# Kernel tuning notes

Hardware: AMD Instinct MI355X
Metric: run time of the kernel (lower is better)

Reference implementation:

```python
import jax, jax.numpy as jnp
import numpy as np

MAX_H = 22
NUM_HEADS = 8
EPS = 1e-5
SLOPE = 0.01  # torch LeakyReLU default


def setup_inputs() -> dict:
    key = jax.random.key(0)
    ks = jax.random.split(key, 8)
    n, c, s, h, w = 16, 64, 30, 64, 22
    cp, v = 64, 17
    p, out_c = 7, 256
    D = c * MAX_H + cp * 2  # fuse_dim = 1536
    sil = jax.random.normal(ks[0], (n, c, s, h, w), dtype=jnp.float32)
    pose = jax.random.normal(ks[1], (n, cp, s, v), dtype=jnp.float32)
    min_idx = jax.random.randint(ks[2], (p, n), 0, h - MAX_H + 1, dtype=jnp.int32)
    max_idx = min_idx + MAX_H  # slices are exactly MAX_H rows (static shape)
    fc_bin = jax.random.normal(ks[3], (p, D, out_c), dtype=jnp.float32) * np.sqrt(2.0 / (D + out_c))
    gamma = 1.0 + 0.1 * jax.random.normal(ks[4], (out_c,), dtype=jnp.float32)
    beta = 0.1 * jax.random.normal(ks[5], (out_c,), dtype=jnp.float32)
    w_qkv = jax.random.normal(ks[6], (3 * out_c, out_c), dtype=jnp.float32) * 0.02
    w_proj = jax.random.normal(ks[7], (out_c, out_c), dtype=jnp.float32) * 0.02
    return {"sil": sil, "pose": pose, "fc_bin": fc_bin, "gamma": gamma, "beta": beta,
            "w_qkv": w_qkv, "w_proj": w_proj, "min_idx": min_idx, "max_idx": max_idx}


def _forward(sil, pose, fc_bin, gamma, beta, w_qkv, w_proj, min_idx):
    n, c, s, h, w = sil.shape
    p = min_idx.shape[0]
    sil_p = jnp.transpose(sil, (0, 2, 1, 3, 4))  # [n,s,c,h,w]
    parts = []
    for j in range(p):  # fixed small part loop; each gather is a big vectorized op
        idx = min_idx[j][:, None] + jnp.arange(MAX_H, dtype=min_idx.dtype)  # [n,MAX_H]
        g = jnp.take_along_axis(sil_p, idx[:, None, None, :, None], axis=3)  # [n,s,c,MAX_H,w]
        parts.append(g.mean(-1) + g.max(-1))  # mean + max pool over width
    silpart = jnp.stack(parts, 0)  # [p,n,s,c,MAX_H]
    silpart = jnp.transpose(silpart, (1, 2, 0, 3, 4)).reshape(n * s, p, c * MAX_H)

    cp, v = pose.shape[1], pose.shape[3]
    pose_r = jnp.transpose(pose, (0, 2, 1, 3)).reshape(n * s, cp, v)  # [ns,cp,17]
    # part 0: AdaptiveAvgPool1d(2) on 5 joints -> mean(j0..j2), mean(j2..j4)
    part0 = jnp.stack([pose_r[:, :, 0:3].mean(-1), pose_r[:, :, 2:5].mean(-1)], -1)  # [ns,cp,2]
    # parts 1..6: pairs of joints, pool(2->2) is identity
    others = pose_r[:, :, 5:].reshape(n * s, cp, 6, 2).transpose(0, 2, 1, 3)  # [ns,6,cp,2]
    posepart = jnp.concatenate([part0[:, None], others], axis=1)  # [ns,p,cp,2]
    posepart = jax.nn.leaky_relu(posepart, SLOPE).reshape(n * s, p, cp * 2)

    fuse = jnp.concatenate([silpart, posepart], axis=2)  # [ns,p,D]
    x = jnp.einsum('npd,pdo->npo', fuse, fc_bin)  # per-part FC -> [ns,p,out]

    # BatchNorm1d (training-mode batch stats) over [ns,out,p]
    x = jnp.transpose(x, (0, 2, 1))  # [ns,out,p]
    mu = x.mean((0, 2), keepdims=True)
    var = x.var((0, 2), keepdims=True)
    x = (x - mu) * jax.lax.rsqrt(var + EPS) * gamma[None, :, None] + beta[None, :, None]
    x = jnp.transpose(x, (0, 2, 1))  # [ns,p,out]

    # Attention over the p part tokens (note: source softmaxes over the HEAD axis)
    B, N, C = x.shape
    hd = C // NUM_HEADS
    qkv = (x @ w_qkv.T).reshape(B, N, 3, NUM_HEADS, hd).transpose(2, 0, 3, 1, 4)
    q, k, vv = qkv[0], qkv[1], qkv[2]  # [B,H,N,hd]
    attn = jnp.einsum('bhnd,bhmd->bhnm', q, k) * (hd ** -0.5)
    attn = jax.nn.softmax(attn, axis=1)  # faithful to attn.softmax(dim=1)
    ao = jnp.einsum('bhnm,bhmd->bhnd', attn, vv).transpose(0, 2, 1, 3).reshape(B, N, C)
    x = x + ao @ w_proj.T

    return x.reshape(n, s, p, C).transpose(0, 3, 1, 2)  # [n,out,s,p]


def reference(sil, pose, fc_bin, gamma, beta, w_qkv, w_proj, min_idx, max_idx):
    # max_idx == min_idx + MAX_H by construction; slice length is static MAX_H
    return _forward(sil, pose, fc_bin, gamma, beta, w_qkv, w_proj, min_idx)
```

## Files before the change

### kernel.cpp

```cpp
#include <hip/hip_runtime.h>
#include <hip/hip_bf16.h>
#include <math.h>

#define NS 480
#define NN 16
#define SS 30
#define CC 64
#define HHH 64
#define WW 22
#define PP 7
#define MAXH 22
#define CP 64
#define VV 17
#define DD 1536
#define OC 256
#define SILD 1408
#define NTOK 3360
#define LDQ 776

typedef __bf16 bf16x8 __attribute__((ext_vector_type(8)));
typedef float f32x4 __attribute__((ext_vector_type(4)));
typedef short short8 __attribute__((ext_vector_type(8)));

__device__ __forceinline__ void gl_lds16(const void* g, void* l) {
    __builtin_amdgcn_global_load_lds(
        (const __attribute__((address_space(1))) void*)g,
        (__attribute__((address_space(3))) void*)l, 16, 0, 0);
}

__device__ __forceinline__ float bf2f(short s) {
    union { float f; unsigned u; } uu; uu.u = ((unsigned)(unsigned short)s) << 16; return uu.f;
}

__global__ __launch_bounds__(256) void prep(const float* __restrict__ sil,
                                            const int* __restrict__ min_idx,
                                            const float* __restrict__ wqkv,
                                            const float* __restrict__ wproj,
                                            const float* __restrict__ fcbin,
                                            const float* __restrict__ pose,
                                            __hip_bfloat16* __restrict__ fuse,
                                            __hip_bfloat16* __restrict__ wqkv16,
                                            __hip_bfloat16* __restrict__ wproj16,
                                            __hip_bfloat16* __restrict__ fcbinT16) {
    __shared__ __align__(16) char smem[47552];
    int b = blockIdx.x, tid = threadIdx.x;
    if (b < 3840) {
        float* lds  = (float*)smem;
        float* hbuf = (float*)(smem + 45056);
        int*   mi_s = (int*)(smem + 47104);
        if (tid < 112) mi_s[tid] = min_idx[tid];
        long long base = (long long)b * 11264;
        int w = tid >> 6, lane = tid & 63;
        const char* gsrc = (const char*)(sil + base) + lane * 16;
        #pragma unroll
        for (int i = 0; i < 11; i++) {
            int ci = w * 11 + i;
            gl_lds16(gsrc + ci * 1024, (char*)smem + ci * 1024);
        }
        __syncthreads();
        #pragma unroll
        for (int rr = 0; rr < 2; rr++) {
            int r = tid + rr * 256;
            const float* row = lds + r * 22;
            float s = 0.f, m = -INFINITY;
            #pragma unroll
            for (int k = 0; k < WW; k++) { float v = row[k]; s += v; m = fmaxf(m, v); }
            hbuf[r] = s * (1.0f / WW) + m;
        }
        __syncthreads();
        int q0 = b * 8;
        for (int idx = tid; idx < 8 * PP * MAXH; idx += 256) {
            int hh = idx % MAXH;
            int t2 = idx / MAXH;
            int j = t2 % PP, qi = t2 / PP;
            int q = q0 + qi;
            int s_i = q % SS, t3 = q / SS;
            int c = t3 & 63, n = t3 >> 6;
            int mi = mi_s[j * NN + n];
            fuse[((long long)(j * NS + n * SS + s_i)) * DD + c * MAXH + hh] =
                __float2bfloat16(hbuf[qi * 64 + mi + hh]);
        }
        return;
    }
    b -= 3840;
    if (b < 768)  { int g = b * 256 + tid; wqkv16[g] = __float2bfloat16(wqkv[g]); return; }
    if (b < 1024) { int g = (b - 768) * 256 + tid; wproj16[g] = __float2bfloat16(wproj[g]); return; }
    if (b < 1696) {
        float (*t)[65] = (float(*)[65])smem;
        int bb = b - 1024;
        int p = bb / 96, r2 = bb % 96, dt = r2 / 4, ot = r2 % 4;
        const float* s = fcbin + ((long long)p * DD + dt * 64) * OC + ot * 64;
        for (int i = tid; i < 64 * 64; i += 256) {
            int r = i >> 6, c = i & 63;
            t[r][c] = s[(long long)r * OC + c];
        }
        __syncthreads();
        __hip_bfloat16* d = fcbinT16 + ((long long)p * OC + ot * 64) * DD + dt * 64;
        for (int i = tid; i < 64 * 64; i += 256) {
            int r = i >> 6, c = i & 63;
            d[(long long)r * DD + c] = __float2bfloat16(t[c][r]);
        }
        return;
    }
    int g = (b - 1696) * 256 + tid;
    int dd = g & 127;
    int t2 = g >> 7;
    int nsi = t2 % NS;
    int j = t2 / NS;
    int n = nsi / SS, s_i = nsi % SS;
    int cpi = dd >> 1, par = dd & 1;
    const float* pr = pose + (((long long)n * CP + cpi) * SS + s_i) * VV;
    float v;
    if (j == 0) {
        v = (par == 0) ? (pr[0] + pr[1] + pr[2]) * (1.f / 3.f)
                       : (pr[2] + pr[3] + pr[4]) * (1.f / 3.f);
    } else {
        v = pr[5 + (j - 1) * 2 + par];
    }
    v = (v > 0.f) ? v : 0.01f * v;
    fuse[(long long)(j * NS + nsi) * DD + SILD + dd] = __float2bfloat16(v);
}

__global__ __launch_bounds__(512) void gemm_fc(
    const __hip_bfloat16* __restrict__ Ain, const __hip_bfloat16* __restrict__ Bt,
    float* __restrict__ Cf, float* __restrict__ partial)
{
    const int M = 480, K = 1536, lda = 1536, ldc = 1792;
    const __hip_bfloat16* Ab = Ain + (long long)blockIdx.z * 480 * 1536;
    const __hip_bfloat16* Bq = Bt + (long long)blockIdx.z * 256 * 1536;
    float* C = Cf + (long long)blockIdx.z * 256;

    __shared__ short As[2][2][4096];
    __shared__ short Bs[2][2][4096];
    __shared__ float red[4][2][16][2];

    int tid = threadIdx.x, lane = tid & 63, w = tid >> 6;
    int kg = w >> 2, wq = w & 3;
    int wm = wq >> 1, wn = wq & 1;
    int row0 = blockIdx.x * 64, col0 = blockIdx.y * 64;
    int kbase = kg * 768;

    f32x4 acc[2][2] = {};

    auto stage = [&](int buf, int k0) {
        int cc = lane & 7;
        #pragma unroll
        for (int i = 0; i < 2; i++) {
            int r = wq * 16 + i * 8 + (lane >> 3);
            int grow = row0 + r; if (grow >= M) grow = M - 1;
            long long kk = kbase + k0;
            const char* ga = (const char*)Ab + (((long long)grow * lda + kk) << 1) + ((cc ^ (r & 7)) << 4);
            gl_lds16(ga, (char*)&As[kg][buf][0] + (wq * 16 + i * 8) * 128);
            const char* gb = (const char*)Bq + (((long long)(col0 + r) * K + kk) << 1) + ((cc ^ (r & 7)) << 4);
            gl_lds16(gb, (char*)&Bs[kg][buf][0] + (wq * 16 + i * 8) * 128);
        }
    };

    stage(0, 0);
    __syncthreads();
    for (int t = 0; t < 12; t++) {
        int cur = t & 1;
        if (t + 1 < 12) stage(cur ^ 1, (t + 1) << 6);
        #pragma unroll
        for (int ks = 0; ks < 2; ks++) {
            bf16x8 af[2], bfv[2];
            #pragma unroll
            for (int f = 0; f < 2; f++) {
                int r = wm * 32 + f * 16 + (lane & 15);
                int ca = (ks * 4 + (lane >> 4)) ^ (r & 7);
                af[f] = *(const bf16x8*)((const char*)&As[kg][cur][0] + r * 128 + (ca << 4));
                int rb = wn * 32 + f * 16 + (lane & 15);
                int cb = (ks * 4 + (lane >> 4)) ^ (rb & 7);
                bfv[f] = *(const bf16x8*)((const char*)&Bs[kg][cur][0] + rb * 128 + (cb << 4));
            }
            #pragma unroll
            for (int fm = 0; fm < 2; fm++)
                #pragma unroll
                for (int fn = 0; fn < 2; fn++)
                    acc[fm][fn] = __builtin_amdgcn_mfma_f32_16x16x32_bf16(
                        af[fm], bfv[fn], acc[fm][fn], 0, 0, 0);
        }
        __syncthreads();
    }

    float* redC = (float*)&As[0][0][0];
    if (kg == 1) {
        #pragma unroll
        for (int fm = 0; fm < 2; fm++)
            #pragma unroll
            for (int fn = 0; fn < 2; fn++)
                #pragma unroll
                for (int r4 = 0; r4 < 4; r4++) {
                    int rl = wm * 32 + fm * 16 + (lane >> 4) * 4 + r4;
                    int cl = wn * 32 + fn * 16 + (lane & 15);
                    redC[rl * 64 + cl] = acc[fm][fn][r4];
                }
    }
    __syncthreads();

    if (kg == 0) {
        float s[2] = {0.f, 0.f}, s2[2] = {0.f, 0.f};
        #pragma unroll
        for (int fm = 0; fm < 2; fm++) {
            #pragma unroll
            for (int fn = 0; fn < 2; fn++) {
                #pragma unroll
                for (int r4 = 0; r4 < 4; r4++) {
                    int rl = wm * 32 + fm * 16 + (lane >> 4) * 4 + r4;
                    int cl = wn * 32 + fn * 16 + (lane & 15);
                    int grow = row0 + rl;
                    if (grow < M) {
                        float v = acc[fm][fn][r4] + redC[rl * 64 + cl];
                        C[(long long)grow * ldc + col0 + cl] = v;
                        s[fn] += v; s2[fn] += v * v;
                    }
                }
            }
        }
        #pragma unroll
        for (int off = 16; off < 64; off <<= 1) {
            s[0] += __shfl_xor(s[0], off);  s2[0] += __shfl_xor(s2[0], off);
            s[1] += __shfl_xor(s[1], off);  s2[1] += __shfl_xor(s2[1], off);
        }
        if (lane < 16) {
            red[wq][0][lane][0] = s[0]; red[wq][0][lane][1] = s2[0];
            red[wq][1][lane][0] = s[1]; red[wq][1][lane][1] = s2[1];
        }
    }
    __syncthreads();
    if (tid < 128) {
        int col = tid >> 1, which = tid & 1;
        int wn2 = (col >> 5) & 1, fn2 = (col >> 4) & 1, c16 = col & 15;
        float v = red[wn2][fn2][c16][which] + red[2 + wn2][fn2][c16][which];
        partial[((long long)(blockIdx.z * 8 + blockIdx.x) * 2 + which) * 256 + blockIdx.y * 64 + col] = v;
    }
}

__global__ __launch_bounds__(256) void bnfinal(const float* __restrict__ partial,
                                               const float* __restrict__ gamma,
                                               const float* __restrict__ beta,
                                               float* __restrict__ ssbuf) {
    int t = threadIdx.x;
    float s = 0.f, s2 = 0.f;
    #pragma unroll 8
    for (int b = 0; b < 56; b++) { s += partial[b * 512 + t]; s2 += partial[b * 512 + 256 + t]; }
    float mu = s / (float)NTOK;
    float var = s2 / (float)NTOK - mu * mu;
    float rsig = rsqrtf(var + 1e-5f);
    float sc = gamma[t] * rsig;
    ssbuf[t] = sc;
    ssbuf[256 + t] = beta[t] - mu * sc;
}

__global__ __launch_bounds__(256) void gemm_qkv(
    const float* __restrict__ xraw, const __hip_bfloat16* __restrict__ Bt,
    const float* __restrict__ ssb, __hip_bfloat16* __restrict__ qkv16)
{
    const int M = 3360, K = 256;
    __shared__ short As[2][4096];
    __shared__ short Bs[2][4096];
    __shared__ float ssl[512];
    int tid = threadIdx.x, lane = tid & 63, w = tid >> 6;
    int wm = w >> 1, wn = w & 1;
    int row0 = blockIdx.x * 64, col0 = blockIdx.y * 64;

    for (int i = tid; i < 512; i += 256) ssl[i] = ssb[i];
    __syncthreads();

    f32x4 acc[2][2] = {};

    auto stageB = [&](int buf, int k0) {
        int cc = lane & 7;
        #pragma unroll
        for (int i = 0; i < 2; i++) {
            int r = w * 16 + i * 8 + (lane >> 3);
            const char* gb = (const char*)Bt + (((long long)(col0 + r) * K + k0) << 1) + ((cc ^ (r & 7)) << 4);
            gl_lds16(gb, (char*)&Bs[buf][0] + (w * 16 + i * 8) * 128);
        }
    };
    auto stageA = [&](int buf, int k0) {
        #pragma unroll
        for (int i = 0; i < 2; i++) {
            int id = tid + i * 256;
            int r = id >> 3, c8 = id & 7;
            int grow = row0 + r; if (grow >= M) grow = M - 1;
            const float* src = xraw + (long long)grow * 256 + k0 + c8 * 8;
            float4 v0 = *(const float4*)src;
            float4 v1 = *(const float4*)(src + 4);
            int kb = k0 + c8 * 8;
            float vv[8] = {v0.x, v0.y, v0.z, v0.w, v1.x, v1.y, v1.z, v1.w};
            short8 o;
            #pragma unroll
            for (int j = 0; j < 8; j++) {
                float tv = vv[j] * ssl[kb + j] + ssl[256 + kb + j];
                union { __hip_bfloat16 h; short s; } u; u.h = __float2bfloat16(tv);
                o[j] = u.s;
            }
            *(short8*)((char*)&As[buf][0] + r * 128 + ((c8 ^ (r & 7)) << 4)) = o;
        }
    };

    stageA(0, 0); stageB(0, 0);
    __syncthreads();
    for (int t = 0; t < 4; t++) {
        int cur = t & 1;
        if (t + 1 < 4) { stageA(cur ^ 1, (t + 1) << 6); stageB(cur ^ 1, (t + 1) << 6); }
        #pragma unroll
        for (int ks = 0; ks < 2; ks++) {
            bf16x8 af[2], bfv[2];
            #pragma unroll
            for (int f = 0; f < 2; f++) {
                int r = wm * 32 + f * 16 + (lane & 15);
                int ca = (ks * 4 + (lane >> 4)) ^ (r & 7);
                af[f] = *(const bf16x8*)((const char*)&As[cur][0] + r * 128 + (ca << 4));
                int rb = wn * 32 + f * 16 + (lane & 15);
                int cb = (ks * 4 + (lane >> 4)) ^ (rb & 7);
                bfv[f] = *(const bf16x8*)((const char*)&Bs[cur][0] + rb * 128 + (cb << 4));
            }
            #pragma unroll
            for (int fm = 0; fm < 2; fm++)
                #pragma unroll
                for (int fn = 0; fn < 2; fn++)
                    acc[fm][fn] = __builtin_amdgcn_mfma_f32_16x16x32_bf16(
                        af[fm], bfv[fn], acc[fm][fn], 0, 0, 0);
        }
        __syncthreads();
    }
    #pragma unroll
    for (int fm = 0; fm < 2; fm++)
        #pragma unroll
        for (int fn = 0; fn < 2; fn++)
            #pragma unroll
            for (int r4 = 0; r4 < 4; r4++) {
                int grow = row0 + wm * 32 + fm * 16 + (lane >> 4) * 4 + r4;
                int gcol = col0 + wn * 32 + fn * 16 + (lane & 15);
                if (grow < M)
                    qkv16[(long long)grow * 768 + gcol] = __float2bfloat16(acc[fm][fn][r4]);
            }
}

__global__ __launch_bounds__(256) void attnproj(const __hip_bfloat16* __restrict__ qkv16,
                                                const __hip_bfloat16* __restrict__ wproj16,
                                                const float* __restrict__ xraw,
                                                const float* __restrict__ ssb,
                                                float* __restrict__ outp) {
    __shared__ __align__(16) char sm[33728];
    float* qkvs = (float*)sm;
    float* Ct   = (float*)sm;
    short* ao_s = (short*)(sm + 21728);
    float (*as_)[49] = (float(*)[49])(sm + 29920);
    float* ssl  = (float*)(sm + 31680);

    int tid = threadIdx.x, lane = tid & 63, w = tid >> 6;
    int token0 = blockIdx.x * 7;

    for (int i = tid; i < 512; i += 256) ssl[i] = ssb[i];

    const short* src = (const short*)qkv16 + (long long)token0 * 768;
    for (int c = tid; c < 672; c += 256) {
        int r = c / 96, c8 = (c % 96) * 8;
        short8 v = *(const short8*)(src + r * 768 + c8);
        float4 f0, f1;
        f0.x = bf2f(v[0]); f0.y = bf2f(v[1]); f0.z = bf2f(v[2]); f0.w = bf2f(v[3]);
        f1.x = bf2f(v[4]); f1.y = bf2f(v[5]); f1.z = bf2f(v[6]); f1.w = bf2f(v[7]);
        *(float4*)&qkvs[r * LDQ + c8] = f0;
        *(float4*)&qkvs[r * LDQ + c8 + 4] = f1;
    }
    __syncthreads();

    for (int t = tid; t < 392; t += 256) {
        int h = t / 49, ij = t % 49, i = ij / 7, j = ij % 7;
        const float* qp = qkvs + i * LDQ + h * 32;
        const float* kp = qkvs + j * LDQ + 256 + h * 32;
        float acc = 0.f;
        #pragma unroll
        for (int d = 0; d < 32; d++) acc += qp[d] * kp[d];
        as_[h][ij] = acc * 0.17677669529663689f;
    }
    __syncthreads();
    if (tid < 49) {
        float m = -INFINITY;
        #pragma unroll
        for (int h = 0; h < 8; h++) m = fmaxf(m, as_[h][tid]);
        float e[8], sum = 0.f;
        #pragma unroll
        for (int h = 0; h < 8; h++) { e[h] = __expf(as_[h][tid] - m); sum += e[h]; }
        float inv = 1.f / sum;
        #pragma unroll
        for (int h = 0; h < 8; h++) as_[h][tid] = e[h] * inv;
    }
    __syncthreads();
    #pragma unroll
    for (int tl = 0; tl < 16; tl++) {
        int col = tid;
        float acc = 0.f;
        if (tl < 7) {
            int h = col >> 5;
            const float* ap = &as_[h][tl * 7];
            const float* vp = qkvs + 512 + col;
            #pragma unroll
            for (int j = 0; j < 7; j++) acc += ap[j] * vp[j * LDQ];
        }
        int c16 = col >> 3;
        union { __hip_bfloat16 h2; short s2; } u; u.h2 = __float2bfloat16(acc);
        ao_s[tl * 256 + ((c16 ^ (tl & 7)) << 3) + (col & 7)] = u.s2;
    }
    __syncthreads();
    f32x4 pacc[4] = {};
    int n0 = w * 64;
    #pragma unroll
    for (int k0 = 0; k0 < 256; k0 += 32) {
        int rowa = lane & 15;
        int kk = k0 + (lane >> 4) * 8;
        int c16a = kk >> 3;
        bf16x8 af = *(const bf16x8*)(const void*)&ao_s[rowa * 256 + ((c16a ^ (rowa & 7)) << 3)];
        #pragma unroll
        for (int fn = 0; fn < 4; fn++) {
            int n = n0 + fn * 16 + (lane & 15);
            bf16x8 bfv = *(const bf16x8*)(const void*)((const short*)wproj16 + n * 256 + kk);
            pacc[fn] = __builtin_amdgcn_mfma_f32_16x16x32_bf16(af, bfv, pacc[fn], 0, 0, 0);
        }
    }
    __syncthreads();
    #pragma unroll
    for (int fn = 0; fn < 4; fn++)
        #pragma unroll
        for (int r4 = 0; r4 < 4; r4++) {
            int tk = (lane >> 4) * 4 + r4;
            if (tk < 7) {
                int o = n0 + fn * 16 + (lane & 15);
                Ct[o * 9 + tk] = pacc[fn][r4];
            }
        }
    __syncthreads();
    int o = tid;
    int n = token0 / 210, rem0 = token0 % 210;
    float* op = outp + ((long long)(n * 256 + o)) * 210 + rem0;
    float sc = ssl[o], sh = ssl[256 + o];
    #pragma unroll
    for (int tk = 0; tk < 7; tk++) {
        op[tk] = Ct[o * 9 + tk] + xraw[(long long)(token0 + tk) * 256 + o] * sc + sh;
    }
}

extern "C" void kernel_launch(void* const* d_in, const int* in_sizes, int n_in,
                              void* d_out, int out_size, void* d_ws, size_t ws_size,
                              hipStream_t stream) {
    const float* sil   = (const float*)d_in[0];
    const float* pose  = (const float*)d_in[1];
    const float* fcbin = (const float*)d_in[2];
    const float* gamma = (const float*)d_in[3];
    const float* beta  = (const float*)d_in[4];
    const float* wqkv  = (const float*)d_in[5];
    const float* wproj = (const float*)d_in[6];
    const int*   minidx= (const int*)d_in[7];
    float* out = (float*)d_out;

    float* ws = (float*)d_ws;
    __hip_bfloat16* fuse16   = (__hip_bfloat16*)ws;
    float* xraw    = ws + 2580480;
    float* partial = ws + 3440640;
    float* ssbuf   = ws + 3469312;
    __hip_bfloat16* wqkv16   = (__hip_bfloat16*)(ws + 3469824);
    __hip_bfloat16* wproj16  = (__hip_bfloat16*)(ws + 3568128);
    __hip_bfloat16* fcbinT16 = (__hip_bfloat16*)(ws + 3600896);
    __hip_bfloat16* qkv16    = (__hip_bfloat16*)(ws + 4977152);

    prep<<<7216, 256, 0, stream>>>(sil, minidx, wqkv, wproj, fcbin, pose,
                                   fuse16, wqkv16, wproj16, fcbinT16);
    gemm_fc<<<dim3(8, 4, 7), 512, 0, stream>>>(fuse16, fcbinT16, xraw, partial);
    bnfinal<<<1, 256, 0, stream>>>(partial, gamma, beta, ssbuf);
    gemm_qkv<<<dim3(53, 12), 256, 0, stream>>>(xraw, wqkv16, ssbuf, qkv16);
    attnproj<<<480, 256, 0, stream>>>(qkv16, wproj16, xraw, ssbuf, out);
}
```

Baseline: 81.43 us.

## Fold BN finalize into QKV GEMM and remap FC GEMM blocks across XCDs

Removes the single-block bnfinal kernel launch. Every gemm_qkv block now reduces the 56 partial BN sums itself to build its scale/shift table, and block (0,0) writes it to global memory for attnproj. The FC GEMM launch is flattened to a 1D grid with a remapped block index, likely so that blocks sharing a part's weights land on the same XCD's L2. The cost is redundant partial-sum reads in all 636 QKV blocks.

```diff
diff --git a/kernel.cpp b/kernel.cpp
--- a/kernel.cpp
+++ b/kernel.cpp
@@ -126,9 +126,15 @@
     float* __restrict__ Cf, float* __restrict__ partial)
 {
     const int M = 480, K = 1536, lda = 1536, ldc = 1792;
-    const __hip_bfloat16* Ab = Ain + (long long)blockIdx.z * 480 * 1536;
-    const __hip_bfloat16* Bq = Bt + (long long)blockIdx.z * 256 * 1536;
-    float* C = Cf + (long long)blockIdx.z * 256;
+    int bid = blockIdx.x;
+    int v = (bid & 7) * 28 + (bid >> 3);
+    int bz = v >> 5;
+    int rem = v & 31;
+    int by = rem >> 3, bx = rem & 7;
+
+    const __hip_bfloat16* Ab = Ain + (long long)bz * 480 * 1536;
+    const __hip_bfloat16* Bq = Bt + (long long)bz * 256 * 1536;
+    float* C = Cf + (long long)bz * 256;
 
     __shared__ short As[2][2][4096];
     __shared__ short Bs[2][2][4096];
@@ -137,7 +143,7 @@
     int tid = threadIdx.x, lane = tid & 63, w = tid >> 6;
     int kg = w >> 2, wq = w & 3;
     int wm = wq >> 1, wn = wq & 1;
-    int row0 = blockIdx.x * 64, col0 = blockIdx.y * 64;
+    int row0 = bx * 64, col0 = by * 64;
     int kbase = kg * 768;
 
     f32x4 acc[2][2] = {};
@@ -210,9 +216,9 @@
                     int cl = wn * 32 + fn * 16 + (lane & 15);
                     int grow = row0 + rl;
                     if (grow < M) {
-                        float v = acc[fm][fn][r4] + redC[rl * 64 + cl];
-                        C[(long long)grow * ldc + col0 + cl] = v;
-                        s[fn] += v; s2[fn] += v * v;
+                        float vv = acc[fm][fn][r4] + redC[rl * 64 + cl];
+                        C[(long long)grow * ldc + col0 + cl] = vv;
+                        s[fn] += vv; s2[fn] += vv * vv;
                     }
                 }
             }
@@ -231,30 +237,16 @@
     if (tid < 128) {
         int col = tid >> 1, which = tid & 1;
         int wn2 = (col >> 5) & 1, fn2 = (col >> 4) & 1, c16 = col & 15;
-        float v = red[wn2][fn2][c16][which] + red[2 + wn2][fn2][c16][which];
-        partial[((long long)(blockIdx.z * 8 + blockIdx.x) * 2 + which) * 256 + blockIdx.y * 64 + col] = v;
-    }
-}
-
-__global__ __launch_bounds__(256) void bnfinal(const float* __restrict__ partial,
-                                               const float* __restrict__ gamma,
-                                               const float* __restrict__ beta,
-                                               float* __restrict__ ssbuf) {
-    int t = threadIdx.x;
-    float s = 0.f, s2 = 0.f;
-    #pragma unroll 8
-    for (int b = 0; b < 56; b++) { s += partial[b * 512 + t]; s2 += partial[b * 512 + 256 + t]; }
-    float mu = s / (float)NTOK;
-    float var = s2 / (float)NTOK - mu * mu;
-    float rsig = rsqrtf(var + 1e-5f);
-    float sc = gamma[t] * rsig;
-    ssbuf[t] = sc;
-    ssbuf[256 + t] = beta[t] - mu * sc;
+        float vv = red[wn2][fn2][c16][which] + red[2 + wn2][fn2][c16][which];
+        partial[((long long)(bz * 8 + bx) * 2 + which) * 256 + by * 64 + col] = vv;
+    }
 }
 
 __global__ __launch_bounds__(256) void gemm_qkv(
     const float* __restrict__ xraw, const __hip_bfloat16* __restrict__ Bt,
-    const float* __restrict__ ssb, __hip_bfloat16* __restrict__ qkv16)
+    const float* __restrict__ partial, const float* __restrict__ gamma,
+    const float* __restrict__ beta, float* __restrict__ ssbuf,
+    __hip_bfloat16* __restrict__ qkv16)
 {
     const int M = 3360, K = 256;
     __shared__ short As[2][4096];
@@ -264,7 +256,25 @@
     int wm = w >> 1, wn = w & 1;
     int row0 = blockIdx.x * 64, col0 = blockIdx.y * 64;
 
-    for (int i = tid; i < 512; i += 256) ssl[i] = ssb[i];
+    {
+        float s = 0.f, s2 = 0.f;
+        #pragma unroll 8
+        for (int bb = 0; bb < 56; bb++) {
+            s  += partial[bb * 512 + tid];
+            s2 += partial[bb * 512 + 256 + tid];
+        }
+        float mu = s * (1.f / NTOK);
+        float var = s2 * (1.f / NTOK) - mu * mu;
+        float rsig = rsqrtf(var + 1e-5f);
+        float sc = gamma[tid] * rsig;
+        float sh = beta[tid] - mu * sc;
+        ssl[tid] = sc;
+        ssl[256 + tid] = sh;
+        if (blockIdx.x == 0 && blockIdx.y == 0) {
+            ssbuf[tid] = sc;
+            ssbuf[256 + tid] = sh;
+        }
+    }
     __syncthreads();
 
     f32x4 acc[2][2] = {};
@@ -468,8 +478,7 @@
 
     prep<<<7216, 256, 0, stream>>>(sil, minidx, wqkv, wproj, fcbin, pose,
                                    fuse16, wqkv16, wproj16, fcbinT16);
-    gemm_fc<<<dim3(8, 4, 7), 512, 0, stream>>>(fuse16, fcbinT16, xraw, partial);
-    bnfinal<<<1, 256, 0, stream>>>(partial, gamma, beta, ssbuf);
-    gemm_qkv<<<dim3(53, 12), 256, 0, stream>>>(xraw, wqkv16, ssbuf, qkv16);
+    gemm_fc<<<224, 512, 0, stream>>>(fuse16, fcbinT16, xraw, partial);
+    gemm_qkv<<<dim3(53, 12), 256, 0, stream>>>(xraw, wqkv16, partial, gamma, beta, ssbuf, qkv16);
     attnproj<<<480, 256, 0, stream>>>(qkv16, wproj16, xraw, ssbuf, out);
 }
```

After: 78.71 us. 3.3% less time.
